# Optimization experiments

Measured on AMD Instinct MI355X. Metric: run time of the kernel, lower is better.

The kernel has to match this reference:

```python
import jax, jax.numpy as jnp
import numpy as np

EMBD_DIM = 768
NUM_HEADS = 12
QKV_DIM = EMBD_DIM // NUM_HEADS  # 64


def setup_inputs() -> dict:
    key = jax.random.key(0)
    k1, k2, k3, k4 = jax.random.split(key, 4)
    B, S = 4, 2048
    X = jax.random.normal(k1, (B, S, EMBD_DIM), dtype=jnp.float32)
    mask = jax.random.randint(k2, (B, S), 0, 2, dtype=jnp.int32)
    scale = 1.0 / np.sqrt(EMBD_DIM)
    W_qkv = jax.random.normal(k3, (EMBD_DIM, 3 * EMBD_DIM), dtype=jnp.float32) * scale
    W_fc = jax.random.normal(k4, (EMBD_DIM, EMBD_DIM), dtype=jnp.float32) * scale
    return {"X": X, "mask": mask, "W_qkv": W_qkv, "W_fc": W_fc}


def reference(X, mask, W_qkv, W_fc):
    B, S, _ = X.shape
    qkv = X @ W_qkv  # (B,S,3*E)
    qkv = qkv.reshape(B, S, NUM_HEADS, 3 * QKV_DIM)
    q, k, v = jnp.split(qkv, 3, axis=-1)  # each (B,S,H,d)
    attn = jnp.einsum('bqhd,bkhd->bhqk', q, k) / np.sqrt(QKV_DIM)
    neg_inf = jnp.finfo(attn.dtype).min
    attn = jnp.where(mask[:, None, None, :] == 0, -jnp.inf, attn)
    attn = jax.nn.softmax(attn, axis=-1)
    out = jnp.einsum('bhqv,bvhd->bqhd', attn, v).reshape(B, S, EMBD_DIM)
    return out @ W_fc
```

## Files before the change

### kernel.cpp

```cpp
#include <hip/hip_runtime.h>
#include <hip/hip_bf16.h>
#include <math.h>

#define NB 4
#define NS 2048
#define NE 768
#define NH 12
#define ND 64
#define NQKV 2304
#define BHN (NB*NH)

typedef __attribute__((ext_vector_type(8))) short bf16x8;
typedef __attribute__((ext_vector_type(4))) float f32x4;
typedef __attribute__((ext_vector_type(16))) float f32x16;
typedef unsigned int uint32;

__device__ __forceinline__ ushort f2bf(float x){
  __hip_bfloat16 h = __float2bfloat16(x);
  return *reinterpret_cast<ushort*>(&h);
}
__device__ __forceinline__ float bf2f(ushort u){
  __hip_bfloat16 h = *reinterpret_cast<__hip_bfloat16*>(&u);
  return __bfloat162float(h);
}
__device__ __forceinline__ void split2(float x, ushort &hi, ushort &lo){
  ushort h = f2bf(x);
  hi = h;
  lo = f2bf(x - bf2f(h));
}
__device__ __forceinline__ uint32 cvtpk(float lo, float hi){
  uint32 r;
  asm("v_cvt_pk_bf16_f32 %0, %1, %2" : "=v"(r) : "v"(lo), "v"(hi));
  return r;
}
__device__ __forceinline__ void pl32swap(uint32 &a, uint32 &b){
  asm("v_permlane32_swap_b32 %0, %1" : "+v"(a), "+v"(b));
}
__device__ __forceinline__ void gl_lds16(const void* g, void* l){
  __builtin_amdgcn_global_load_lds(
      (const __attribute__((address_space(1))) unsigned int*)g,
      (__attribute__((address_space(3))) unsigned int*)l, 16, 0, 0);
}
__device__ __forceinline__ f32x16 zero16(){
  f32x16 z;
#pragma unroll
  for (int i=0;i<16;++i) z[i] = 0.f;
  return z;
}

__global__ __launch_bounds__(256)
void k_convert_x(const float* __restrict__ X, ushort* __restrict__ H, ushort* __restrict__ L)
{
  const int idx = (blockIdx.x*256 + threadIdx.x)*8;
  float4 x0 = *(const float4*)(X+idx);
  float4 x1 = *(const float4*)(X+idx+4);
  float xs[8] = {x0.x,x0.y,x0.z,x0.w,x1.x,x1.y,x1.z,x1.w};
  bf16x8 vh, vl;
#pragma unroll
  for (int i=0;i<8;++i){
    ushort hi, lo; split2(xs[i], hi, lo);
    vh[i] = (short)hi; vl[i] = (short)lo;
  }
  *(bf16x8*)(H+idx) = vh;
  *(bf16x8*)(L+idx) = vl;
}

__global__ __launch_bounds__(256)
void k_transpose_w(const float* __restrict__ W, ushort* __restrict__ TH, ushort* __restrict__ TL,
                   int K, int N)
{
  __shared__ ushort LH[64][72], LL[64][72];
  const int tid = threadIdx.x;
  const int k0 = blockIdx.y*64, n0 = blockIdx.x*64;
  const int kk = tid >> 4, nn = (tid & 15)*4;
#pragma unroll
  for (int p=0;p<4;++p){
    const int k = kk + p*16;
    float4 v = *(const float4*)(W + (size_t)(k0+k)*N + n0 + nn);
    float xs[4] = {v.x, v.y, v.z, v.w};
#pragma unroll
    for (int c=0;c<4;++c){
      ushort hi, lo; split2(xs[c], hi, lo);
      LH[nn+c][k] = hi; LL[nn+c][k] = lo;
    }
  }
  __syncthreads();
  const int nr = tid >> 2, ch = (tid & 3)*16;
  bf16x8 h0, h1, l0, l1;
#pragma unroll
  for (int i=0;i<8;++i){
    h0[i] = (short)LH[nr][ch+i];   h1[i] = (short)LH[nr][ch+8+i];
    l0[i] = (short)LL[nr][ch+i];   l1[i] = (short)LL[nr][ch+8+i];
  }
  ushort* dh = TH + (size_t)(n0+nr)*K + k0 + ch;
  ushort* dl = TL + (size_t)(n0+nr)*K + k0 + ch;
  *(bf16x8*)dh = h0; *(bf16x8*)(dh+8) = h1;
  *(bf16x8*)dl = l0; *(bf16x8*)(dl+8) = l1;
}

__global__ __launch_bounds__(256)
void k_maskprep(const int* __restrict__ mask, uint32* __restrict__ MW)
{
  const int tid = threadIdx.x;
  const int b = tid >> 6, kt = (tid >> 1) & 31, h = tid & 1;
  uint32 wv = 0;
#pragma unroll
  for (int t=0;t<2;++t){
#pragma unroll
    for (int r=0;r<16;++r){
      const int key = (r&3) + 8*(r>>2) + 4*h + 32*t;
      if (mask[b*NS + kt*64 + key] != 0) wv |= (1u << (r + 16*t));
    }
  }
  MW[tid] = wv;
}

template<int MODE, int NT>
__global__ __launch_bounds__(256)
void k_gemm(const ushort* __restrict__ Ah, const ushort* __restrict__ Al,
            const ushort* __restrict__ Bh, const ushort* __restrict__ Bl,
            float* __restrict__ C,
            ushort* __restrict__ Qo, ushort* __restrict__ Ko, ushort* __restrict__ Vo,
            int M, int N, int K)
{
  __shared__ ushort Ash[128][40], Asl[128][40], Bsh[128][40], Bsl[128][40];
  const int tid = threadIdx.x;
  const int lane = tid & 63;
  const int w = tid >> 6;
  const int wm = w & 1, wn = w >> 1;
  const int l15 = lane & 15, lg = lane >> 4;
  const int m0 = blockIdx.y*128, n0 = blockIdx.x*128;

  f32x4 acc[4][4] = {};

  const int sr  = tid >> 1;
  const int scc = (tid & 1)*16;

  for (int k0 = 0; k0 < K; k0 += 32) {
    if (k0) __syncthreads();
    {
      const size_t ao = (size_t)(m0+sr)*K + k0 + scc;
      bf16x8 ah0 = *(const bf16x8*)(Ah+ao), ah1 = *(const bf16x8*)(Ah+ao+8);
      bf16x8 al0 = *(const bf16x8*)(Al+ao), al1 = *(const bf16x8*)(Al+ao+8);
      const size_t bo = (size_t)(n0+sr)*K + k0 + scc;
      bf16x8 bh0 = *(const bf16x8*)(Bh+bo), bh1 = *(const bf16x8*)(Bh+bo+8);
      *(bf16x8*)&Ash[sr][scc] = ah0; *(bf16x8*)&Ash[sr][scc+8] = ah1;
      *(bf16x8*)&Asl[sr][scc] = al0; *(bf16x8*)&Asl[sr][scc+8] = al1;
      *(bf16x8*)&Bsh[sr][scc] = bh0; *(bf16x8*)&Bsh[sr][scc+8] = bh1;
      if (NT == 3) {
        bf16x8 bl0 = *(const bf16x8*)(Bl+bo), bl1 = *(const bf16x8*)(Bl+bo+8);
        *(bf16x8*)&Bsl[sr][scc] = bl0; *(bf16x8*)&Bsl[sr][scc+8] = bl1;
      }
    }
    __syncthreads();

    bf16x8 fah[4], fal[4], fbh[4], fbl[4];
#pragma unroll
    for (int i=0;i<4;++i){
      fah[i] = *(const bf16x8*)&Ash[wm*64 + i*16 + l15][lg*8];
      fal[i] = *(const bf16x8*)&Asl[wm*64 + i*16 + l15][lg*8];
      fbh[i] = *(const bf16x8*)&Bsh[wn*64 + i*16 + l15][lg*8];
      if (NT == 3) fbl[i] = *(const bf16x8*)&Bsl[wn*64 + i*16 + l15][lg*8];
    }
#pragma unroll
    for (int mi=0;mi<4;++mi){
#pragma unroll
      for (int ni=0;ni<4;++ni){
        acc[mi][ni] = __builtin_amdgcn_mfma_f32_16x16x32_bf16(fah[mi], fbh[ni], acc[mi][ni], 0,0,0);
        if (NT == 3)
          acc[mi][ni] = __builtin_amdgcn_mfma_f32_16x16x32_bf16(fah[mi], fbl[ni], acc[mi][ni], 0,0,0);
        acc[mi][ni] = __builtin_amdgcn_mfma_f32_16x16x32_bf16(fal[mi], fbh[ni], acc[mi][ni], 0,0,0);
      }
    }
  }

#pragma unroll
  for (int mi=0;mi<4;++mi){
#pragma unroll
    for (int ni=0;ni<4;++ni){
#pragma unroll
      for (int j=0;j<4;++j){
        const int m = m0 + wm*64 + mi*16 + lg*4 + j;
        const int n = n0 + wn*64 + ni*16 + l15;
        const float v = acc[mi][ni][j];
        if (MODE == 0) {
          const int bb = m >> 11, ss = m & 2047;
          const int hh = n / 192, rr = n - hh*192;
          const int d = rr & 63;
          if (rr < 128) {
            ushort* dst = (rr < 64) ? Qo : Ko;
            dst[((size_t)(bb*NH + hh)*NS + ss)*ND + d] = f2bf(v);
          } else {
            Vo[((size_t)(bb*NH + hh)*ND + d)*NS + ss] = f2bf(v);
          }
        } else {
          C[(size_t)m*N + n] = v;
        }
      }
    }
  }
}

__global__ __launch_bounds__(256)
void k_attn(const ushort* __restrict__ Qb, const ushort* __restrict__ Kb,
            const ushort* __restrict__ VTb, const uint32* __restrict__ MW,
            ushort* __restrict__ Ohi, ushort* __restrict__ Olo)
{
  __shared__ ushort Kls[2][4096];
  __shared__ ushort Vls[2][4096];

  const int tid = threadIdx.x;
  const int lane = tid & 63;
  const int w = tid >> 6;
  const int l31 = lane & 31;
  const int h = lane >> 5;
  const int qt = blockIdx.x, head = blockIdx.y, b = blockIdx.z;
  const int bh = b*NH + head;
  const int qglob = qt*128 + w*32 + l31;

  bf16x8 qf[4];
  {
    const ushort* qp = Qb + ((size_t)bh*NS + qglob)*ND + h*8;
#pragma unroll
    for (int s=0;s<4;++s) qf[s] = *(const bf16x8*)(qp + s*16);
  }

  const int srow = (w<<3) + (lane>>3);
  const int scol = ((lane&7) ^ (lane>>3)) << 3;
  const ushort* Kg  = Kb  + (size_t)bh*NS*ND;
  const ushort* VTg = VTb + (size_t)bh*ND*NS;
  const int lbase = (w<<9);

#define STAGE(kt_, bsel_)                                                     \
  {                                                                           \
    _Pragma("unroll")                                                         \
    for (int i_=0;i_<2;++i_){                                                 \
      const int row_ = i_*32 + srow;                                          \
      gl_lds16(Kg  + (size_t)((kt_)*64 + row_)*ND + scol,                     \
               &Kls[bsel_][i_*2048 + lbase]);                                 \
      gl_lds16(VTg + (size_t)row_*NS + (kt_)*64 + scol,                       \
               &Vls[bsel_][i_*2048 + lbase]);                                 \
    }                                                                         \
  }

  f32x16 o0 = zero16(), o1 = zero16();
  float m_run = -INFINITY, l_run = 0.f;

  STAGE(0, 0);
  __syncthreads();

  for (int kt = 0; kt < NS/64; ++kt){
    const int buf = kt & 1;
    if (kt + 1 < NS/64) STAGE(kt+1, buf^1);
    const uint32 mw = MW[b*64 + kt*2 + h];

    f32x16 z0 = zero16(), z1 = zero16();
    const char* kbase = (const char*)&Kls[buf][0];
#pragma unroll
    for (int s=0;s<4;++s){
      const int cb = (s*32 + h*16) ^ ((l31&7)<<4);
      bf16x8 kf0 = *(const bf16x8*)(kbase + l31*128 + cb);
      z0 = __builtin_amdgcn_mfma_f32_32x32x16_bf16(kf0, qf[s], z0, 0,0,0);
      bf16x8 kf1 = *(const bf16x8*)(kbase + (32+l31)*128 + cb);
      z1 = __builtin_amdgcn_mfma_f32_32x32x16_bf16(kf1, qf[s], z1, 0,0,0);
    }

    float sc[32];
    float tmax = -INFINITY;
#pragma unroll
    for (int r=0;r<16;++r){
      float s0 = z0[r]*0.125f;
      s0 = (mw & (1u<<r)) ? s0 : -INFINITY;
      sc[r] = s0;
      float s1 = z1[r]*0.125f;
      s1 = (mw & (1u<<(16+r))) ? s1 : -INFINITY;
      sc[16+r] = s1;
      tmax = fmaxf(tmax, fmaxf(s0, s1));
    }
    tmax = fmaxf(tmax, __shfl_xor(tmax, 32));
    const float mnew  = fmaxf(m_run, tmax);
    const float msafe = fmaxf(mnew, -1e30f);
    const float alpha = __expf(m_run - msafe);
    float psum = 0.f;
#pragma unroll
    for (int r=0;r<32;++r){
      float p = __expf(sc[r] - msafe);
      sc[r] = p;
      psum += p;
    }
    psum += __shfl_xor(psum, 32);
    l_run = l_run*alpha + psum;
    m_run = mnew;
#pragma unroll
    for (int r=0;r<16;++r){ o0[r] *= alpha; o1[r] *= alpha; }

    const char* vbase = (const char*)&Vls[buf][0];
#pragma unroll
    for (int ks=0;ks<4;++ks){
      const int rb = (ks&1)*8 + (ks>>1)*16;
      uint32 d0 = cvtpk(sc[rb+0], sc[rb+1]);
      uint32 d2 = cvtpk(sc[rb+4], sc[rb+5]);
      pl32swap(d0, d2);
      uint32 d1 = cvtpk(sc[rb+2], sc[rb+3]);
      uint32 d3 = cvtpk(sc[rb+6], sc[rb+7]);
      pl32swap(d1, d3);
      union { uint32 u[4]; bf16x8 v; } pf;
      pf.u[0] = d0; pf.u[1] = d1; pf.u[2] = d2; pf.u[3] = d3;
      const int cb = (ks*32 + h*16) ^ ((l31&7)<<4);
      bf16x8 vf0 = *(const bf16x8*)(vbase + l31*128 + cb);
      o0 = __builtin_amdgcn_mfma_f32_32x32x16_bf16(vf0, pf.v, o0, 0,0,0);
      bf16x8 vf1 = *(const bf16x8*)(vbase + (32+l31)*128 + cb);
      o1 = __builtin_amdgcn_mfma_f32_32x32x16_bf16(vf1, pf.v, o1, 0,0,0);
    }
    __syncthreads();
  }

  const float inv = 1.f / l_run;
  const size_t obase = ((size_t)(b*NS + qglob))*NE + head*ND;
#pragma unroll
  for (int a=0;a<2;++a){
#pragma unroll
    for (int rp=0;rp<8;++rp){
      const int r = rp*2;
      const float v0 = (a ? o1[r]   : o0[r])   * inv;
      const float v1 = (a ? o1[r+1] : o0[r+1]) * inv;
      ushort h0,lo0,h1,lo1;
      split2(v0, h0, lo0); split2(v1, h1, lo1);
      const int d = (r&3) + 8*(r>>2) + 4*h + 32*a;
      *(uint32*)(Ohi + obase + d) = (uint32)h0 | ((uint32)h1<<16);
      *(uint32*)(Olo + obase + d) = (uint32)lo0 | ((uint32)lo1<<16);
    }
  }
#undef STAGE
}

extern "C" void kernel_launch(void* const* d_in, const int* in_sizes, int n_in,
                              void* d_out, int out_size, void* d_ws, size_t ws_size,
                              hipStream_t stream)
{
  const float* X    = (const float*)d_in[0];
  const int*   mask = (const int*)d_in[1];
  const float* Wqkv = (const float*)d_in[2];
  const float* Wfc  = (const float*)d_in[3];
  float* out = (float*)d_out;

  char* p = (char*)d_ws;
  const size_t szXE = (size_t)NB*NS*NE;
  const size_t szT  = (size_t)BHN*NS*ND;
  ushort* Xhi = (ushort*)p; p += szXE*2;
  ushort* Xlo = (ushort*)p; p += szXE*2;
  ushort* Wqh = (ushort*)p; p += (size_t)NQKV*NE*2;
  ushort* Wql = (ushort*)p; p += (size_t)NQKV*NE*2;
  ushort* Wfh = (ushort*)p; p += (size_t)NE*NE*2;
  ushort* Wfl = (ushort*)p; p += (size_t)NE*NE*2;
  ushort* Qb  = (ushort*)p; p += szT*2;
  ushort* Kb  = (ushort*)p; p += szT*2;
  ushort* VTb = (ushort*)p; p += szT*2;
  ushort* Ohi = (ushort*)p; p += szXE*2;
  ushort* Olo = (ushort*)p; p += szXE*2;
  uint32* MW  = (uint32*)p; p += 256*4;

  k_convert_x<<<(int)(szXE/2048), 256, 0, stream>>>(X, Xhi, Xlo);
  k_transpose_w<<<dim3(NQKV/64, NE/64), 256, 0, stream>>>(Wqkv, Wqh, Wql, NE, NQKV);
  k_transpose_w<<<dim3(NE/64, NE/64), 256, 0, stream>>>(Wfc, Wfh, Wfl, NE, NE);
  k_maskprep<<<1, 256, 0, stream>>>(mask, MW);
  k_gemm<0,2><<<dim3(NQKV/128, (NB*NS)/128), 256, 0, stream>>>(
      Xhi, Xlo, Wqh, Wql, nullptr, Qb, Kb, VTb, NB*NS, NQKV, NE);
  k_attn<<<dim3(NS/128, NH, NB), 256, 0, stream>>>(Qb, Kb, VTb, MW, Ohi, Olo);
  k_gemm<1,3><<<dim3(NE/128, (NB*NS)/128), 256, 0, stream>>>(
      Ohi, Olo, Wfh, Wfl, out, nullptr, nullptr, nullptr, NB*NS, NE, NE);
}
```

Before: 351.0 us.

## Use direct-to-LDS loads in GEMM, fold softmax scale into Q, lazy rescale

The GEMM now stages tiles with global_load_lds into XOR-swizzled LDS instead of going through registers. The QKV epilogue pre-multiplies Q by 0.125*log2(e), so attention can use exp2f with no per-score scaling. The mask is applied by initialising the MFMA accumulator to -FLT_MAX where keys are masked, and the running-max rescale of O and l is skipped when no lane's max grew. s_setprio raises wave priority around the MFMA blocks. This trims VALU work per tile and register-path staging, at the cost of more complex swizzle indexing and a slight change in where rounding happens for Q.

```diff
diff --git a/kernel.cpp b/kernel.cpp
--- a/kernel.cpp
+++ b/kernel.cpp
@@ -15,6 +15,8 @@
 typedef __attribute__((ext_vector_type(16))) float f32x16;
 typedef unsigned int uint32;
 
+#define QSCALE (0.125f * 1.44269504f)
+
 __device__ __forceinline__ ushort f2bf(float x){
   __hip_bfloat16 h = __float2bfloat16(x);
   return *reinterpret_cast<ushort*>(&h);
@@ -40,12 +42,6 @@
   __builtin_amdgcn_global_load_lds(
       (const __attribute__((address_space(1))) unsigned int*)g,
       (__attribute__((address_space(3))) unsigned int*)l, 16, 0, 0);
-}
-__device__ __forceinline__ f32x16 zero16(){
-  f32x16 z;
-#pragma unroll
-  for (int i=0;i<16;++i) z[i] = 0.f;
-  return z;
 }
 
 __global__ __launch_bounds__(256)
@@ -123,7 +119,8 @@
             ushort* __restrict__ Qo, ushort* __restrict__ Ko, ushort* __restrict__ Vo,
             int M, int N, int K)
 {
-  __shared__ ushort Ash[128][40], Asl[128][40], Bsh[128][40], Bsl[128][40];
+  __shared__ ushort Ash[4096], Asl[4096], Bsh[4096];
+  __shared__ ushort Bsl[NT == 3 ? 4096 : 16];
   const int tid = threadIdx.x;
   const int lane = tid & 63;
   const int w = tid >> 6;
@@ -133,35 +130,38 @@
 
   f32x4 acc[4][4] = {};
 
-  const int sr  = tid >> 1;
-  const int scc = (tid & 1)*16;
+  const int srow   = tid >> 2;
+  const int schunk = tid & 3;
+  const int ldst   = tid*8;
 
   for (int k0 = 0; k0 < K; k0 += 32) {
     if (k0) __syncthreads();
-    {
-      const size_t ao = (size_t)(m0+sr)*K + k0 + scc;
-      bf16x8 ah0 = *(const bf16x8*)(Ah+ao), ah1 = *(const bf16x8*)(Ah+ao+8);
-      bf16x8 al0 = *(const bf16x8*)(Al+ao), al1 = *(const bf16x8*)(Al+ao+8);
-      const size_t bo = (size_t)(n0+sr)*K + k0 + scc;
-      bf16x8 bh0 = *(const bf16x8*)(Bh+bo), bh1 = *(const bf16x8*)(Bh+bo+8);
-      *(bf16x8*)&Ash[sr][scc] = ah0; *(bf16x8*)&Ash[sr][scc+8] = ah1;
-      *(bf16x8*)&Asl[sr][scc] = al0; *(bf16x8*)&Asl[sr][scc+8] = al1;
-      *(bf16x8*)&Bsh[sr][scc] = bh0; *(bf16x8*)&Bsh[sr][scc+8] = bh1;
-      if (NT == 3) {
-        bf16x8 bl0 = *(const bf16x8*)(Bl+bo), bl1 = *(const bf16x8*)(Bl+bo+8);
-        *(bf16x8*)&Bsl[sr][scc] = bl0; *(bf16x8*)&Bsl[sr][scc+8] = bl1;
-      }
+#pragma unroll
+    for (int i=0;i<2;++i){
+      const int row = i*64 + srow;
+      const int kc  = (schunk ^ ((row>>1)&3))*8;
+      const size_t ao = (size_t)(m0+row)*K + k0 + kc;
+      const size_t bo = (size_t)(n0+row)*K + k0 + kc;
+      gl_lds16(Ah+ao, &Ash[i*2048+ldst]);
+      gl_lds16(Al+ao, &Asl[i*2048+ldst]);
+      gl_lds16(Bh+bo, &Bsh[i*2048+ldst]);
+      if (NT == 3) gl_lds16(Bl+bo, &Bsl[i*2048+ldst]);
     }
     __syncthreads();
 
     bf16x8 fah[4], fal[4], fbh[4], fbl[4];
 #pragma unroll
     for (int i=0;i<4;++i){
-      fah[i] = *(const bf16x8*)&Ash[wm*64 + i*16 + l15][lg*8];
-      fal[i] = *(const bf16x8*)&Asl[wm*64 + i*16 + l15][lg*8];
-      fbh[i] = *(const bf16x8*)&Bsh[wn*64 + i*16 + l15][lg*8];
-      if (NT == 3) fbl[i] = *(const bf16x8*)&Bsl[wn*64 + i*16 + l15][lg*8];
-    }
+      const int ra = wm*64 + i*16 + l15;
+      const int ca = (lg ^ ((ra>>1)&3))*8;
+      fah[i] = *(const bf16x8*)&Ash[ra*32 + ca];
+      fal[i] = *(const bf16x8*)&Asl[ra*32 + ca];
+      const int rb = wn*64 + i*16 + l15;
+      const int cb = (lg ^ ((rb>>1)&3))*8;
+      fbh[i] = *(const bf16x8*)&Bsh[rb*32 + cb];
+      if (NT == 3) fbl[i] = *(const bf16x8*)&Bsl[rb*32 + cb];
+    }
+    __builtin_amdgcn_s_setprio(1);
 #pragma unroll
     for (int mi=0;mi<4;++mi){
 #pragma unroll
@@ -172,6 +172,7 @@
         acc[mi][ni] = __builtin_amdgcn_mfma_f32_16x16x32_bf16(fal[mi], fbh[ni], acc[mi][ni], 0,0,0);
       }
     }
+    __builtin_amdgcn_s_setprio(0);
   }
 
 #pragma unroll
@@ -180,16 +181,17 @@
     for (int ni=0;ni<4;++ni){
 #pragma unroll
       for (int j=0;j<4;++j){
-        const int m = m0 + wm*64 + mi*16 + lg*4 + j;
+        const int m = m0 + wm*64 + mi*16 + (lane>>4)*4 + j;
         const int n = n0 + wn*64 + ni*16 + l15;
         const float v = acc[mi][ni][j];
         if (MODE == 0) {
           const int bb = m >> 11, ss = m & 2047;
           const int hh = n / 192, rr = n - hh*192;
           const int d = rr & 63;
-          if (rr < 128) {
-            ushort* dst = (rr < 64) ? Qo : Ko;
-            dst[((size_t)(bb*NH + hh)*NS + ss)*ND + d] = f2bf(v);
+          if (rr < 64) {
+            Qo[((size_t)(bb*NH + hh)*NS + ss)*ND + d] = f2bf(v * QSCALE);
+          } else if (rr < 128) {
+            Ko[((size_t)(bb*NH + hh)*NS + ss)*ND + d] = f2bf(v);
           } else {
             Vo[((size_t)(bb*NH + hh)*ND + d)*NS + ss] = f2bf(v);
           }
@@ -243,7 +245,9 @@
     }                                                                         \
   }
 
-  f32x16 o0 = zero16(), o1 = zero16();
+  f32x16 o0, o1;
+#pragma unroll
+  for (int r=0;r<16;++r){ o0[r]=0.f; o1[r]=0.f; }
   float m_run = -INFINITY, l_run = 0.f;
 
   STAGE(0, 0);
@@ -254,8 +258,17 @@
     if (kt + 1 < NS/64) STAGE(kt+1, buf^1);
     const uint32 mw = MW[b*64 + kt*2 + h];
 
-    f32x16 z0 = zero16(), z1 = zero16();
+    f32x16 z0, z1;
+#pragma unroll
+    for (int r=0;r<16;++r){
+      const int b0 = ((int)(mw << (31-r))) >> 31;
+      const int b1 = ((int)(mw << (15-r))) >> 31;
+      z0[r] = __int_as_float(~b0 & 0xFF7FFFFFu);
+      z1[r] = __int_as_float(~b1 & 0xFF7FFFFFu);
+    }
+
     const char* kbase = (const char*)&Kls[buf][0];
+    __builtin_amdgcn_s_setprio(1);
 #pragma unroll
     for (int s=0;s<4;++s){
       const int cb = (s*32 + h*16) ^ ((l31&7)<<4);
@@ -264,35 +277,35 @@
       bf16x8 kf1 = *(const bf16x8*)(kbase + (32+l31)*128 + cb);
       z1 = __builtin_amdgcn_mfma_f32_32x32x16_bf16(kf1, qf[s], z1, 0,0,0);
     }
+    __builtin_amdgcn_s_setprio(0);
+
+    float tmax = fmaxf(z0[0], z1[0]);
+#pragma unroll
+    for (int r=1;r<16;++r) tmax = fmaxf(tmax, fmaxf(z0[r], z1[r]));
+    tmax = fmaxf(tmax, __shfl_xor(tmax, 32));
+
+    if (!__all(tmax <= m_run)) {
+      const float mnew  = fmaxf(m_run, tmax);
+      const float msafe = fmaxf(mnew, -1e30f);
+      const float alpha = exp2f(m_run - msafe);
+      m_run = mnew;
+      l_run *= alpha;
+#pragma unroll
+      for (int r=0;r<16;++r){ o0[r] *= alpha; o1[r] *= alpha; }
+    }
+    const float mbase = fmaxf(m_run, -1e30f);
 
     float sc[32];
-    float tmax = -INFINITY;
+    float psum = 0.f;
 #pragma unroll
     for (int r=0;r<16;++r){
-      float s0 = z0[r]*0.125f;
-      s0 = (mw & (1u<<r)) ? s0 : -INFINITY;
-      sc[r] = s0;
-      float s1 = z1[r]*0.125f;
-      s1 = (mw & (1u<<(16+r))) ? s1 : -INFINITY;
-      sc[16+r] = s1;
-      tmax = fmaxf(tmax, fmaxf(s0, s1));
-    }
-    tmax = fmaxf(tmax, __shfl_xor(tmax, 32));
-    const float mnew  = fmaxf(m_run, tmax);
-    const float msafe = fmaxf(mnew, -1e30f);
-    const float alpha = __expf(m_run - msafe);
-    float psum = 0.f;
-#pragma unroll
-    for (int r=0;r<32;++r){
-      float p = __expf(sc[r] - msafe);
-      sc[r] = p;
-      psum += p;
+      const float p0 = exp2f(z0[r] - mbase);
+      const float p1 = exp2f(z1[r] - mbase);
+      sc[r] = p0; sc[16+r] = p1;
+      psum += p0 + p1;
     }
     psum += __shfl_xor(psum, 32);
-    l_run = l_run*alpha + psum;
-    m_run = mnew;
-#pragma unroll
-    for (int r=0;r<16;++r){ o0[r] *= alpha; o1[r] *= alpha; }
+    l_run += psum;
 
     const char* vbase = (const char*)&Vls[buf][0];
 #pragma unroll
@@ -307,10 +320,12 @@
       union { uint32 u[4]; bf16x8 v; } pf;
       pf.u[0] = d0; pf.u[1] = d1; pf.u[2] = d2; pf.u[3] = d3;
       const int cb = (ks*32 + h*16) ^ ((l31&7)<<4);
+      __builtin_amdgcn_s_setprio(1);
       bf16x8 vf0 = *(const bf16x8*)(vbase + l31*128 + cb);
       o0 = __builtin_amdgcn_mfma_f32_32x32x16_bf16(vf0, pf.v, o0, 0,0,0);
       bf16x8 vf1 = *(const bf16x8*)(vbase + (32+l31)*128 + cb);
       o1 = __builtin_amdgcn_mfma_f32_32x32x16_bf16(vf1, pf.v, o1, 0,0,0);
+      __builtin_amdgcn_s_setprio(0);
     }
     __syncthreads();
   }
```

Result: slower. 378.6 us (+7.9%).
